# Kernel optimization log

Hardware: AMD Instinct MI355X
Metric: run time of the kernel (lower is better)

Reference implementation:

```python
import jax, jax.numpy as jnp
import numpy as np

B, T, D, H = 4, 2048, 1024, 16
E = D // H  # 64
DH = D // 4  # sensor hidden dim


def setup_inputs() -> dict:
    key = jax.random.key(0)
    ks = jax.random.split(key, 9)
    s = D ** -0.5
    return {
        "x": jax.random.normal(ks[0], (B, T, D), jnp.float32),
        "q_w": jax.random.normal(ks[1], (D, D), jnp.float32) * s,
        "k_w": jax.random.normal(ks[2], (D, D), jnp.float32) * s,
        "v_w": jax.random.normal(ks[3], (D, D), jnp.float32) * s,
        "o_w": jax.random.normal(ks[4], (D, D), jnp.float32) * s,
        "cs_w1": jax.random.normal(ks[5], (DH, D), jnp.float32) * s,
        "cs_b1": jnp.zeros((DH,), jnp.float32),
        "cs_w2": jax.random.normal(ks[6], (H, DH), jnp.float32) * (DH ** -0.5),
        "cs_b2": jnp.zeros((H,), jnp.float32),
        "decay_params": jax.random.normal(ks[7], (H, E), jnp.float32) + 3.0,
    }


def reference(x, q_w, k_w, v_w, o_w, cs_w1, cs_b1, cs_w2, cs_b2, decay_params):
    Bx, Tx, Dx = x.shape
    # projections (torch Linear: y = x @ W.T), split into heads
    q = (x @ q_w.T).reshape(Bx, Tx, H, E)
    k = (x @ k_w.T).reshape(Bx, Tx, H, E)
    v = (x @ v_w.T).reshape(Bx, Tx, H, E)
    # complexity sensor -> per-head scalar in (0,1)
    lc = jax.nn.sigmoid(jnp.tanh(x @ cs_w1.T + cs_b1) @ cs_w2.T + cs_b2)  # [B,T,H]
    base = jax.nn.sigmoid(decay_params)[None, None]                       # [1,1,H,E]
    lam = jnp.clip(base * (1.0 + 0.2 * lc[..., None]), 0.0, 0.9995)       # [B,T,H,E]

    def step(state, inp):
        qt, kt, vt, dt = inp  # each [B,H,E]
        # S(t) = diag(dt) S(t-1) + k_t v_t^T  (decay along key dim e)
        state = state * dt[..., None] + kt[..., None] * vt[:, :, None, :]
        out_t = jnp.einsum('bhe,bhef->bhf', qt, state)
        return state, out_t

    init = jnp.zeros((Bx, H, E, E), x.dtype)
    xs = (jnp.swapaxes(q, 0, 1), jnp.swapaxes(k, 0, 1),
          jnp.swapaxes(v, 0, 1), jnp.swapaxes(lam, 0, 1))  # time-major
    _, ys = jax.lax.scan(step, init, xs)  # ys: [T,B,H,E]
    y = jnp.swapaxes(ys, 0, 1).reshape(Bx, Tx, Dx)
    return y @ o_w.T
```

## Files before the change

### kernel.cpp

```cpp
#include <hip/hip_runtime.h>

#define DEV __device__ __forceinline__
#define MFMA(a, b, c) __builtin_amdgcn_mfma_f32_16x16x32_bf16(a, b, c, 0, 0, 0)

typedef __bf16 bf16x8 __attribute__((ext_vector_type(8)));
typedef float f32x4 __attribute__((ext_vector_type(4)));
typedef unsigned short u16x8 __attribute__((ext_vector_type(8)));

DEV float blo(unsigned u) { return __builtin_bit_cast(float, u << 16); }
DEV float bhi(unsigned u) { return __builtin_bit_cast(float, u & 0xFFFF0000u); }
DEV unsigned short f2b(float f) {
  unsigned u = __builtin_bit_cast(unsigned, f);
  return (unsigned short)((u + 0x7FFFu + ((u >> 16) & 1u)) >> 16);
}
DEV float sigf(float x) { return 1.0f / (1.0f + expf(-x)); }

DEV void llds16(const void* g, void* l) {
  __builtin_amdgcn_global_load_lds(
      (__attribute__((address_space(1))) void*)(void*)g,
      (__attribute__((address_space(3))) void*)l, 16, 0, 0);
}

__global__ __launch_bounds__(256) void cvt_all_kernel(
    const float* __restrict__ x, const float* __restrict__ qw,
    const float* __restrict__ kw, const float* __restrict__ vw,
    const float* __restrict__ cw1, const float* __restrict__ ow,
    unsigned short* __restrict__ XB, unsigned short* __restrict__ WCAT,
    unsigned short* __restrict__ OWB) {
  const int i = blockIdx.x * 256 + threadIdx.x;
  const float* s;
  unsigned short* d;
  if (i < 2097152)      { s = x   + (size_t)i * 4;                 d = XB + (size_t)i * 4; }
  else if (i < 2359296) { size_t j = i - 2097152; s = qw  + j * 4; d = WCAT + j * 4; }
  else if (i < 2621440) { size_t j = i - 2359296; s = kw  + j * 4; d = WCAT + 1048576 + j * 4; }
  else if (i < 2883584) { size_t j = i - 2621440; s = vw  + j * 4; d = WCAT + 2097152 + j * 4; }
  else if (i < 2949120) { size_t j = i - 2883584; s = cw1 + j * 4; d = WCAT + 3145728 + j * 4; }
  else if (i < 3211264) { size_t j = i - 2949120; s = ow  + j * 4; d = OWB + j * 4; }
  else return;
  float4 f = *(const float4*)s;
  ushort4 o;
  o.x = f2b(f.x); o.y = f2b(f.y); o.z = f2b(f.z); o.w = f2b(f.w);
  *(ushort4*)d = o;
}

template <int OUTF>
__global__ __launch_bounds__(256, 2) void gemm_bk64_kernel(
    const unsigned short* __restrict__ A, const unsigned short* __restrict__ B,
    void* __restrict__ Cout, int M, int N, int K, int act_col0,
    const float* __restrict__ bias, int nbn) {
  __shared__ char As[16384];
  __shared__ char Bs[16384];
  const int tid = threadIdx.x;
  const int lane = tid & 63;
  const int w = tid >> 6;
  const int wr = w >> 1, wc = w & 1;
  const int ln15 = lane & 15, hi = lane >> 4;

  const int nwg = gridDim.x, orig = blockIdx.x;
  const int qd = nwg >> 3, rm = nwg & 7;
  const int xcd = orig & 7, loc = orig >> 3;
  const int swz = (xcd < rm ? xcd * (qd + 1) : rm * (qd + 1) + (xcd - rm) * qd) + loc;
  const int bn = swz % nbn, bm = swz / nbn;
  const int m0 = bm * 128, n0 = bn * 128;

  auto stage = [&](const unsigned short* src, int row0, int k0, char* dst) {
#pragma unroll
    for (int j = 0; j < 4; ++j) {
      const int slot = j * 256 + tid;
      const int rr = slot >> 3;
      const int kc = (slot & 7) ^ (rr & 7);
      llds16(src + (size_t)(row0 + rr) * K + k0 + kc * 8, dst + slot * 16);
    }
  };
  auto rd = [&](const char* unit, int row, int ks) -> bf16x8 {
    const int kc = (ks * 4 + hi) ^ (row & 7);
    return *(const bf16x8*)(unit + row * 128 + kc * 16);
  };

  f32x4 acc[4][4] = {};
  const int nk = K >> 6;
  for (int kt = 0; kt < nk; ++kt) {
    stage(A, m0, kt * 64, As);
    stage(B, n0, kt * 64, Bs);
    __syncthreads();
    bf16x8 af[2][4], bf[2][4];
#pragma unroll
    for (int ks = 0; ks < 2; ++ks)
#pragma unroll
      for (int i = 0; i < 4; ++i) {
        af[ks][i] = rd(As, wr * 64 + i * 16 + ln15, ks);
        bf[ks][i] = rd(Bs, wc * 64 + i * 16 + ln15, ks);
      }
#pragma unroll
    for (int i = 0; i < 4; ++i)
#pragma unroll
      for (int j = 0; j < 4; ++j) {
        acc[i][j] = MFMA(af[0][i], bf[0][j], acc[i][j]);
        acc[i][j] = MFMA(af[1][i], bf[1][j], acc[i][j]);
      }
    __syncthreads();
  }
#pragma unroll
  for (int i = 0; i < 4; ++i) {
    const int rowb = m0 + wr * 64 + i * 16 + hi * 4;
#pragma unroll
    for (int j = 0; j < 4; ++j) {
      const int col = n0 + wc * 64 + j * 16 + ln15;
#pragma unroll
      for (int r = 0; r < 4; ++r) {
        float v = acc[i][j][r];
        if (col >= act_col0) v = tanhf(v + bias[col - act_col0]);
        const size_t off = (size_t)(rowb + r) * N + col;
        if (OUTF == 0) ((unsigned short*)Cout)[off] = f2b(v);
        else ((float*)Cout)[off] = v;
      }
    }
  }
}

__global__ __launch_bounds__(256) void sensor2_kernel(
    const unsigned short* __restrict__ QKVH, const float* __restrict__ w2,
    const float* __restrict__ b2, float* __restrict__ LC) {
  const int tid = threadIdx.x;
  const int h = tid & 15, r = tid >> 4;
  const int m = blockIdx.x * 16 + r;
  const unsigned short* hrow = QKVH + (size_t)m * 3328 + 3072;
  const float* wrow = w2 + h * 256;
  float acc = 0.0f;
  for (int d = 0; d < 256; d += 8) {
    uint4 hv = *(const uint4*)(hrow + d);
    float4 wa = *(const float4*)(wrow + d);
    float4 wb = *(const float4*)(wrow + d + 4);
    acc = fmaf(blo(hv.x), wa.x, acc); acc = fmaf(bhi(hv.x), wa.y, acc);
    acc = fmaf(blo(hv.y), wa.z, acc); acc = fmaf(bhi(hv.y), wa.w, acc);
    acc = fmaf(blo(hv.z), wb.x, acc); acc = fmaf(bhi(hv.z), wb.y, acc);
    acc = fmaf(blo(hv.w), wb.z, acc); acc = fmaf(bhi(hv.w), wb.w, acc);
  }
  LC[(size_t)m * 16 + h] = sigf(acc + b2[h]);
}

__global__ __launch_bounds__(256) void scan_passA_kernel(
    const unsigned short* __restrict__ QKVH, const float* __restrict__ LC,
    const float* __restrict__ decay, float* __restrict__ MT, float* __restrict__ P) {
  __shared__ char SH[34304];
  ushort* kL = (ushort*)SH;
  ushort* vL = (ushort*)(SH + 8192);
  char* khT  = SH + 16384;
  char* vT   = SH + 24576;
  float* sigL = (float*)(SH + 32768);
  float* lcL  = (float*)(SH + 33024);
  float* Lp   = (float*)(SH + 33280);

  const int tid = threadIdx.x;
  const int c = blockIdx.x, h = blockIdx.y, b = blockIdx.z;
  const int t0 = c * 64;
#pragma unroll
  for (int i = 0; i < 2; ++i) {
    int idx = i * 256 + tid;
    int row = idx >> 3, ch = idx & 7;
    size_t g = (size_t)(b * 2048 + t0 + row) * 3328 + h * 64 + ch * 8;
    int lb = (i * 256 + (tid >> 6) * 64) * 16;
    llds16(QKVH + g + 1024, (char*)kL + lb);
    llds16(QKVH + g + 2048, (char*)vL + lb);
  }
  if (tid < 64) sigL[tid] = sigf(decay[h * 64 + tid]);
  else if (tid < 128) lcL[tid - 64] = LC[(size_t)(b * 2048 + t0 + tid - 64) * 16 + h];
  __syncthreads();

  const int e = tid & 63, seg = tid >> 6;
  const float sig_e = sigL[e];
  float lp = 1.f;
#pragma unroll
  for (int i = 0; i < 16; ++i)
    lp *= fminf(sig_e * (1.f + 0.2f * lcL[seg * 16 + i]), 0.9995f);
  Lp[seg * 64 + e] = lp;
  __syncthreads();
  float T = 1.f;
#pragma unroll
  for (int sg = 0; sg < 4; ++sg) if (sg > seg) T *= Lp[sg * 64 + e];

  u16x8 ka = {}, kb = {};
  float r = T;
#pragma unroll
  for (int i = 15; i >= 0; --i) {
    int s = seg * 16 + i;
    float lam = fminf(sig_e * (1.f + 0.2f * lcL[s]), 0.9995f);
    float kv = blo((unsigned)kL[s * 64 + e]) * r;
    if (i >= 8) kb[i - 8] = f2b(kv); else ka[i] = f2b(kv);
    r *= lam;
  }
  *(u16x8*)(khT + e * 128 + (((2 * seg + 0) ^ (e & 7)) * 16)) = ka;
  *(u16x8*)(khT + e * 128 + (((2 * seg + 1) ^ (e & 7)) * 16)) = kb;
  if (seg == 0) P[((size_t)((b * 16 + h) * 32 + c)) * 64 + e] = r;

  u16x8 va = {}, vb = {};
#pragma unroll
  for (int i = 0; i < 16; ++i) {
    unsigned short vv = vL[(seg * 16 + i) * 64 + e];
    if (i >= 8) vb[i - 8] = vv; else va[i] = vv;
  }
  *(u16x8*)(vT + e * 128 + (((2 * seg + 0) ^ (e & 7)) * 16)) = va;
  *(u16x8*)(vT + e * 128 + (((2 * seg + 1) ^ (e & 7)) * 16)) = vb;
  __syncthreads();

  const int ln15 = tid & 15, hi = (tid & 63) >> 4, w = tid >> 6;
  auto rd = [&](const char* u, int row, int ks) -> bf16x8 {
    return *(const bf16x8*)(u + row * 128 + (((ks * 4 + hi) ^ (row & 7)) * 16));
  };
  bf16x8 av0 = rd(vT, w * 16 + ln15, 0), av1 = rd(vT, w * 16 + ln15, 1);
  float* Mp = MT + ((size_t)((b * 16 + h) * 32 + c)) * 4096;
#pragma unroll
  for (int er = 0; er < 4; ++er) {
    f32x4 acc = {};
    acc = MFMA(av0, rd(khT, er * 16 + ln15, 0), acc);
    acc = MFMA(av1, rd(khT, er * 16 + ln15, 1), acc);
#pragma unroll
    for (int rr = 0; rr < 4; ++rr)
      Mp[(w * 16 + hi * 4 + rr) * 64 + er * 16 + ln15] = acc[rr];
  }
}

__global__ __launch_bounds__(256) void scan_passB_kernel(
    float* __restrict__ MT, const float* __restrict__ P) {
  const int bh = blockIdx.y;
  const int ef = blockIdx.x * 256 + threadIdx.x;
  const int e = ef & 63;
  const size_t base = (size_t)bh * 32;
  float S = 0.0f;
  for (int c = 0; c < 32; ++c) {
    float* Mp = MT + (base + c) * 4096 + ef;
    const float p = P[(base + c) * 64 + e];
    const float m = *Mp;
    *Mp = S;
    S = fmaf(p, S, m);
  }
}

__global__ __launch_bounds__(256) void scan_passC_kernel(
    const unsigned short* __restrict__ QKVH, const float* __restrict__ LC,
    const float* __restrict__ decay, const float* __restrict__ MT,
    unsigned short* __restrict__ Y) {
  __shared__ char SH[50688];
  ushort* qL = (ushort*)SH;
  ushort* kL = (ushort*)(SH + 8192);
  ushort* vL = (ushort*)(SH + 16384);
  char* qT = SH + 24576;
  char* kT = SH + 32768;
  char* vT = SH + 40960;
  char* Ab   = SH;
  char* sinT = SH + 8192;
  float* sigL = (float*)(SH + 49152);
  float* lcL  = (float*)(SH + 49408);
  float* Lp   = (float*)(SH + 49664);

  const int tid = threadIdx.x;
  const int c = blockIdx.x, h = blockIdx.y, b = blockIdx.z;
  const int t0 = c * 64;
#pragma unroll
  for (int i = 0; i < 2; ++i) {
    int idx = i * 256 + tid;
    int row = idx >> 3, ch = idx & 7;
    size_t g = (size_t)(b * 2048 + t0 + row) * 3328 + h * 64 + ch * 8;
    int lb = (i * 256 + (tid >> 6) * 64) * 16;
    llds16(QKVH + g,        (char*)qL + lb);
    llds16(QKVH + g + 1024, (char*)kL + lb);
    llds16(QKVH + g + 2048, (char*)vL + lb);
  }
  if (tid < 64) sigL[tid] = sigf(decay[h * 64 + tid]);
  else if (tid < 128) lcL[tid - 64] = LC[(size_t)(b * 2048 + t0 + tid - 64) * 16 + h];
  __syncthreads();

  const int e = tid & 63, seg = tid >> 6;
  const float sig_e = sigL[e];
  float lp = 1.f;
#pragma unroll
  for (int i = 0; i < 16; ++i)
    lp *= fminf(sig_e * (1.f + 0.2f * lcL[seg * 16 + i]), 0.9995f);
  Lp[seg * 64 + e] = lp;
  __syncthreads();
  float a = 1.f;
#pragma unroll
  for (int sg = 0; sg < 4; ++sg) if (sg < seg) a *= Lp[sg * 64 + e];

#pragma unroll
  for (int i = 0; i < 16; ++i) {
    int t = seg * 16 + i;
    a *= fminf(sig_e * (1.f + 0.2f * lcL[t]), 0.9995f);
    float qv = blo((unsigned)qL[t * 64 + e]) * a;
    float kv = blo((unsigned)kL[t * 64 + e]) / fmaxf(a, 1e-30f);
    int off = ((e >> 3) ^ (t & 7)) * 16 + (e & 7) * 2;
    *(unsigned short*)(qT + t * 128 + off) = f2b(qv);
    *(unsigned short*)(kT + t * 128 + off) = f2b(kv);
  }
  u16x8 va = {}, vb = {};
#pragma unroll
  for (int i = 0; i < 16; ++i) {
    unsigned short vv = vL[(seg * 16 + i) * 64 + e];
    if (i >= 8) vb[i - 8] = vv; else va[i] = vv;
  }
  *(u16x8*)(vT + e * 128 + (((2 * seg + 0) ^ (e & 7)) * 16)) = va;
  *(u16x8*)(vT + e * 128 + (((2 * seg + 1) ^ (e & 7)) * 16)) = vb;
  __syncthreads();

  const int ln15 = tid & 15, hi = (tid & 63) >> 4, w = tid >> 6;
  auto rd = [&](const char* u, int row, int ks) -> bf16x8 {
    return *(const bf16x8*)(u + row * 128 + (((ks * 4 + hi) ^ (row & 7)) * 16));
  };
  bf16x8 Aq0 = rd(qT, w * 16 + ln15, 0), Aq1 = rd(qT, w * 16 + ln15, 1);
  f32x4 acc1[4];
#pragma unroll
  for (int sr = 0; sr < 4; ++sr) {
    acc1[sr] = (f32x4){0.f, 0.f, 0.f, 0.f};
    if (sr <= w) {
      acc1[sr] = MFMA(Aq0, rd(kT, sr * 16 + ln15, 0), acc1[sr]);
      acc1[sr] = MFMA(Aq1, rd(kT, sr * 16 + ln15, 1), acc1[sr]);
    }
  }
#pragma unroll
  for (int sr = 0; sr < 4; ++sr)
#pragma unroll
    for (int rr = 0; rr < 4; ++rr) {
      int t = w * 16 + hi * 4 + rr;
      int s = sr * 16 + ln15;
      float v = 0.f;
      if (sr <= w && s <= t) v = acc1[sr][rr];
      *(unsigned short*)(Ab + t * 128 + (((s >> 3) ^ (t & 7)) * 16) + (s & 7) * 2) = f2b(v);
    }
  {
    const float* Ms = MT + ((size_t)((b * 16 + h) * 32 + c)) * 4096 + (tid >> 2) * 64 + (tid & 3) * 16;
    const int f2 = tid >> 2, s0 = (tid & 3) * 2;
    u16x8 sa = {}, sb = {};
#pragma unroll
    for (int j = 0; j < 4; ++j) {
      float4 m4 = *(const float4*)(Ms + j * 4);
      if (j < 2) {
        sa[j * 4 + 0] = f2b(m4.x); sa[j * 4 + 1] = f2b(m4.y);
        sa[j * 4 + 2] = f2b(m4.z); sa[j * 4 + 3] = f2b(m4.w);
      } else {
        sb[(j - 2) * 4 + 0] = f2b(m4.x); sb[(j - 2) * 4 + 1] = f2b(m4.y);
        sb[(j - 2) * 4 + 2] = f2b(m4.z); sb[(j - 2) * 4 + 3] = f2b(m4.w);
      }
    }
    *(u16x8*)(sinT + f2 * 128 + (((s0 + 0) ^ (f2 & 7)) * 16)) = sa;
    *(u16x8*)(sinT + f2 * 128 + (((s0 + 1) ^ (f2 & 7)) * 16)) = sb;
  }
  __syncthreads();

  f32x4 accY[4];
#pragma unroll
  for (int fr = 0; fr < 4; ++fr) {
    accY[fr] = (f32x4){0.f, 0.f, 0.f, 0.f};
    accY[fr] = MFMA(Aq0, rd(sinT, fr * 16 + ln15, 0), accY[fr]);
    accY[fr] = MFMA(Aq1, rd(sinT, fr * 16 + ln15, 1), accY[fr]);
  }
  bf16x8 Aa0 = rd(Ab, w * 16 + ln15, 0), Aa1 = rd(Ab, w * 16 + ln15, 1);
#pragma unroll
  for (int fr = 0; fr < 4; ++fr) {
    accY[fr] = MFMA(Aa0, rd(vT, fr * 16 + ln15, 0), accY[fr]);
    accY[fr] = MFMA(Aa1, rd(vT, fr * 16 + ln15, 1), accY[fr]);
  }
#pragma unroll
  for (int fr = 0; fr < 4; ++fr)
#pragma unroll
    for (int rr = 0; rr < 4; ++rr)
      Y[(size_t)(b * 2048 + t0 + w * 16 + hi * 4 + rr) * 1024 + h * 64 + fr * 16 + ln15]
        = f2b(accY[fr][rr]);
}

extern "C" void kernel_launch(void* const* d_in, const int* in_sizes, int n_in,
                              void* d_out, int out_size, void* d_ws, size_t ws_size,
                              hipStream_t stream) {
  (void)in_sizes; (void)n_in; (void)out_size; (void)ws_size;
  const float* x     = (const float*)d_in[0];
  const float* q_w   = (const float*)d_in[1];
  const float* k_w   = (const float*)d_in[2];
  const float* v_w   = (const float*)d_in[3];
  const float* o_w   = (const float*)d_in[4];
  const float* cs_w1 = (const float*)d_in[5];
  const float* cs_b1 = (const float*)d_in[6];
  const float* cs_w2 = (const float*)d_in[7];
  const float* cs_b2 = (const float*)d_in[8];
  const float* decay = (const float*)d_in[9];
  float* out = (float*)d_out;

  char* ws = (char*)d_ws;
  unsigned short* XB   = (unsigned short*)(ws);
  unsigned short* WCAT = (unsigned short*)(ws + 16777216);
  unsigned short* OWB  = (unsigned short*)(ws + 23592960);
  unsigned short* QKVH = (unsigned short*)(ws + 25690112);
  float*          LCb  = (float*)(ws + 80216064);
  float*          MT   = (float*)(ws + 80740352);
  float*          Pb   = (float*)(ws + 114294784);
  unsigned short* YB   = (unsigned short*)(ws + 114819072);

  cvt_all_kernel<<<12544, 256, 0, stream>>>(x, q_w, k_w, v_w, cs_w1, o_w,
                                            XB, WCAT, OWB);

  gemm_bk64_kernel<0><<<1664, 256, 0, stream>>>(XB, WCAT, QKVH, 8192, 3328,
                                                1024, 3072, cs_b1, 26);
  sensor2_kernel<<<512, 256, 0, stream>>>(QKVH, cs_w2, cs_b2, LCb);

  scan_passA_kernel<<<dim3(32, 16, 4), 256, 0, stream>>>(QKVH, LCb, decay, MT, Pb);
  scan_passB_kernel<<<dim3(16, 64), 256, 0, stream>>>(MT, Pb);
  scan_passC_kernel<<<dim3(32, 16, 4), 256, 0, stream>>>(QKVH, LCb, decay, MT, YB);

  gemm_bk64_kernel<1><<<512, 256, 0, stream>>>(YB, OWB, out, 8192, 1024,
                                               1024, 1 << 30, nullptr, 8);
}
```

Baseline: 174.5 us.

## Store inter-chunk states as swizzled bf16 and split sensor hidden output

Pass A now writes the per-chunk state contributions as bf16 in the XOR-swizzled LDS layout instead of fp32. Pass B carries the prefix scan in fp32 but reads and writes bf16, and pass C pulls the states straight into LDS with async global-to-LDS loads, dropping its per-thread fp32 load and convert. The QKV GEMM writes the tanh sensor columns to a separate 256-wide buffer, so QKV rows are 3072 wide. This halves the state traffic and removes conversion work, at the cost of extra rounding: the prefix states are stored in bf16 between chunks.

```diff
diff --git a/kernel.cpp b/kernel.cpp
--- a/kernel.cpp
+++ b/kernel.cpp
@@ -46,8 +46,8 @@
 template <int OUTF>
 __global__ __launch_bounds__(256, 2) void gemm_bk64_kernel(
     const unsigned short* __restrict__ A, const unsigned short* __restrict__ B,
-    void* __restrict__ Cout, int M, int N, int K, int act_col0,
-    const float* __restrict__ bias, int nbn) {
+    void* __restrict__ Cout, unsigned short* __restrict__ Cout2,
+    int K, int ldC, int act_col0, const float* __restrict__ bias, int nbn) {
   __shared__ char As[16384];
   __shared__ char Bs[16384];
   const int tid = threadIdx.x;
@@ -109,22 +109,26 @@
 #pragma unroll
       for (int r = 0; r < 4; ++r) {
         float v = acc[i][j][r];
-        if (col >= act_col0) v = tanhf(v + bias[col - act_col0]);
-        const size_t off = (size_t)(rowb + r) * N + col;
-        if (OUTF == 0) ((unsigned short*)Cout)[off] = f2b(v);
-        else ((float*)Cout)[off] = v;
+        if (col >= act_col0) {
+          v = tanhf(v + bias[col - act_col0]);
+          Cout2[(size_t)(rowb + r) * 256 + (col - act_col0)] = f2b(v);
+        } else {
+          const size_t off = (size_t)(rowb + r) * ldC + col;
+          if (OUTF == 0) ((unsigned short*)Cout)[off] = f2b(v);
+          else ((float*)Cout)[off] = v;
+        }
       }
     }
   }
 }
 
 __global__ __launch_bounds__(256) void sensor2_kernel(
-    const unsigned short* __restrict__ QKVH, const float* __restrict__ w2,
+    const unsigned short* __restrict__ H1, const float* __restrict__ w2,
     const float* __restrict__ b2, float* __restrict__ LC) {
   const int tid = threadIdx.x;
   const int h = tid & 15, r = tid >> 4;
   const int m = blockIdx.x * 16 + r;
-  const unsigned short* hrow = QKVH + (size_t)m * 3328 + 3072;
+  const unsigned short* hrow = H1 + (size_t)m * 256;
   const float* wrow = w2 + h * 256;
   float acc = 0.0f;
   for (int d = 0; d < 256; d += 8) {
@@ -140,8 +144,9 @@
 }
 
 __global__ __launch_bounds__(256) void scan_passA_kernel(
-    const unsigned short* __restrict__ QKVH, const float* __restrict__ LC,
-    const float* __restrict__ decay, float* __restrict__ MT, float* __restrict__ P) {
+    const unsigned short* __restrict__ QKV, const float* __restrict__ LC,
+    const float* __restrict__ decay, unsigned short* __restrict__ MTB,
+    float* __restrict__ P) {
   __shared__ char SH[34304];
   ushort* kL = (ushort*)SH;
   ushort* vL = (ushort*)(SH + 8192);
@@ -158,10 +163,10 @@
   for (int i = 0; i < 2; ++i) {
     int idx = i * 256 + tid;
     int row = idx >> 3, ch = idx & 7;
-    size_t g = (size_t)(b * 2048 + t0 + row) * 3328 + h * 64 + ch * 8;
+    size_t g = (size_t)(b * 2048 + t0 + row) * 3072 + h * 64 + ch * 8;
     int lb = (i * 256 + (tid >> 6) * 64) * 16;
-    llds16(QKVH + g + 1024, (char*)kL + lb);
-    llds16(QKVH + g + 2048, (char*)vL + lb);
+    llds16(QKV + g + 1024, (char*)kL + lb);
+    llds16(QKV + g + 2048, (char*)vL + lb);
   }
   if (tid < 64) sigL[tid] = sigf(decay[h * 64 + tid]);
   else if (tid < 128) lcL[tid - 64] = LC[(size_t)(b * 2048 + t0 + tid - 64) * 16 + h];
@@ -208,37 +213,41 @@
     return *(const bf16x8*)(u + row * 128 + (((ks * 4 + hi) ^ (row & 7)) * 16));
   };
   bf16x8 av0 = rd(vT, w * 16 + ln15, 0), av1 = rd(vT, w * 16 + ln15, 1);
-  float* Mp = MT + ((size_t)((b * 16 + h) * 32 + c)) * 4096;
+  unsigned short* Mp = MTB + ((size_t)((b * 16 + h) * 32 + c)) * 4096;
 #pragma unroll
   for (int er = 0; er < 4; ++er) {
     f32x4 acc = {};
     acc = MFMA(av0, rd(khT, er * 16 + ln15, 0), acc);
     acc = MFMA(av1, rd(khT, er * 16 + ln15, 1), acc);
-#pragma unroll
-    for (int rr = 0; rr < 4; ++rr)
-      Mp[(w * 16 + hi * 4 + rr) * 64 + er * 16 + ln15] = acc[rr];
+    const int e2 = er * 16 + ln15;
+#pragma unroll
+    for (int rr = 0; rr < 4; ++rr) {
+      const int f = w * 16 + hi * 4 + rr;
+      Mp[f * 64 + (((e2 >> 3) ^ (f & 7)) << 3) + (e2 & 7)] = f2b(acc[rr]);
+    }
   }
 }
 
 __global__ __launch_bounds__(256) void scan_passB_kernel(
-    float* __restrict__ MT, const float* __restrict__ P) {
+    unsigned short* __restrict__ MTB, const float* __restrict__ P) {
   const int bh = blockIdx.y;
-  const int ef = blockIdx.x * 256 + threadIdx.x;
-  const int e = ef & 63;
+  const int task = blockIdx.x * 256 + threadIdx.x;
+  const int f = task >> 6, slot = (task >> 3) & 7, pos = task & 7;
+  const int e = ((slot ^ (f & 7)) << 3) | pos;
   const size_t base = (size_t)bh * 32;
   float S = 0.0f;
   for (int c = 0; c < 32; ++c) {
-    float* Mp = MT + (base + c) * 4096 + ef;
+    unsigned short* Mp = MTB + (base + c) * 4096 + task;
     const float p = P[(base + c) * 64 + e];
-    const float m = *Mp;
-    *Mp = S;
+    const float m = blo((unsigned)*Mp);
+    *Mp = f2b(S);
     S = fmaf(p, S, m);
   }
 }
 
 __global__ __launch_bounds__(256) void scan_passC_kernel(
-    const unsigned short* __restrict__ QKVH, const float* __restrict__ LC,
-    const float* __restrict__ decay, const float* __restrict__ MT,
+    const unsigned short* __restrict__ QKV, const float* __restrict__ LC,
+    const float* __restrict__ decay, const unsigned short* __restrict__ MTB,
     unsigned short* __restrict__ Y) {
   __shared__ char SH[50688];
   ushort* qL = (ushort*)SH;
@@ -260,11 +269,11 @@
   for (int i = 0; i < 2; ++i) {
     int idx = i * 256 + tid;
     int row = idx >> 3, ch = idx & 7;
-    size_t g = (size_t)(b * 2048 + t0 + row) * 3328 + h * 64 + ch * 8;
+    size_t g = (size_t)(b * 2048 + t0 + row) * 3072 + h * 64 + ch * 8;
     int lb = (i * 256 + (tid >> 6) * 64) * 16;
-    llds16(QKVH + g,        (char*)qL + lb);
-    llds16(QKVH + g + 1024, (char*)kL + lb);
-    llds16(QKVH + g + 2048, (char*)vL + lb);
+    llds16(QKV + g,        (char*)qL + lb);
+    llds16(QKV + g + 1024, (char*)kL + lb);
+    llds16(QKV + g + 2048, (char*)vL + lb);
   }
   if (tid < 64) sigL[tid] = sigf(decay[h * 64 + tid]);
   else if (tid < 128) lcL[tid - 64] = LC[(size_t)(b * 2048 + t0 + tid - 64) * 16 + h];
@@ -302,6 +311,12 @@
   *(u16x8*)(vT + e * 128 + (((2 * seg + 1) ^ (e & 7)) * 16)) = vb;
   __syncthreads();
 
+  {
+    const unsigned short* Ms = MTB + ((size_t)((b * 16 + h) * 32 + c)) * 4096;
+#pragma unroll
+    for (int i = 0; i < 2; ++i)
+      llds16(Ms + (size_t)(i * 256 + tid) * 8, sinT + (i * 256 + (tid >> 6) * 64) * 16);
+  }
   const int ln15 = tid & 15, hi = (tid & 63) >> 4, w = tid >> 6;
   auto rd = [&](const char* u, int row, int ks) -> bf16x8 {
     return *(const bf16x8*)(u + row * 128 + (((ks * 4 + hi) ^ (row & 7)) * 16));
@@ -326,24 +341,7 @@
       if (sr <= w && s <= t) v = acc1[sr][rr];
       *(unsigned short*)(Ab + t * 128 + (((s >> 3) ^ (t & 7)) * 16) + (s & 7) * 2) = f2b(v);
     }
-  {
-    const float* Ms = MT + ((size_t)((b * 16 + h) * 32 + c)) * 4096 + (tid >> 2) * 64 + (tid & 3) * 16;
-    const int f2 = tid >> 2, s0 = (tid & 3) * 2;
-    u16x8 sa = {}, sb = {};
-#pragma unroll
-    for (int j = 0; j < 4; ++j) {
-      float4 m4 = *(const float4*)(Ms + j * 4);
-      if (j < 2) {
-        sa[j * 4 + 0] = f2b(m4.x); sa[j * 4 + 1] = f2b(m4.y);
-        sa[j * 4 + 2] = f2b(m4.z); sa[j * 4 + 3] = f2b(m4.w);
-      } else {
-        sb[(j - 2) * 4 + 0] = f2b(m4.x); sb[(j - 2) * 4 + 1] = f2b(m4.y);
-        sb[(j - 2) * 4 + 2] = f2b(m4.z); sb[(j - 2) * 4 + 3] = f2b(m4.w);
-      }
-    }
-    *(u16x8*)(sinT + f2 * 128 + (((s0 + 0) ^ (f2 & 7)) * 16)) = sa;
-    *(u16x8*)(sinT + f2 * 128 + (((s0 + 1) ^ (f2 & 7)) * 16)) = sb;
-  }
+  bf16x8 Aa0 = rd(Ab, w * 16 + ln15, 0), Aa1 = rd(Ab, w * 16 + ln15, 1);
   __syncthreads();
 
   f32x4 accY[4];
@@ -352,10 +350,6 @@
     accY[fr] = (f32x4){0.f, 0.f, 0.f, 0.f};
     accY[fr] = MFMA(Aq0, rd(sinT, fr * 16 + ln15, 0), accY[fr]);
     accY[fr] = MFMA(Aq1, rd(sinT, fr * 16 + ln15, 1), accY[fr]);
-  }
-  bf16x8 Aa0 = rd(Ab, w * 16 + ln15, 0), Aa1 = rd(Ab, w * 16 + ln15, 1);
-#pragma unroll
-  for (int fr = 0; fr < 4; ++fr) {
     accY[fr] = MFMA(Aa0, rd(vT, fr * 16 + ln15, 0), accY[fr]);
     accY[fr] = MFMA(Aa1, rd(vT, fr * 16 + ln15, 1), accY[fr]);
   }
@@ -387,23 +381,24 @@
   unsigned short* XB   = (unsigned short*)(ws);
   unsigned short* WCAT = (unsigned short*)(ws + 16777216);
   unsigned short* OWB  = (unsigned short*)(ws + 23592960);
-  unsigned short* QKVH = (unsigned short*)(ws + 25690112);
+  unsigned short* QKV  = (unsigned short*)(ws + 25690112);
+  unsigned short* H1   = (unsigned short*)(ws + 76021760);
   float*          LCb  = (float*)(ws + 80216064);
-  float*          MT   = (float*)(ws + 80740352);
-  float*          Pb   = (float*)(ws + 114294784);
-  unsigned short* YB   = (unsigned short*)(ws + 114819072);
+  unsigned short* MTB  = (unsigned short*)(ws + 80740352);
+  float*          Pb   = (float*)(ws + 97517568);
+  unsigned short* YB   = (unsigned short*)(ws + 98041856);
 
   cvt_all_kernel<<<12544, 256, 0, stream>>>(x, q_w, k_w, v_w, cs_w1, o_w,
                                             XB, WCAT, OWB);
 
-  gemm_bk64_kernel<0><<<1664, 256, 0, stream>>>(XB, WCAT, QKVH, 8192, 3328,
-                                                1024, 3072, cs_b1, 26);
-  sensor2_kernel<<<512, 256, 0, stream>>>(QKVH, cs_w2, cs_b2, LCb);
-
-  scan_passA_kernel<<<dim3(32, 16, 4), 256, 0, stream>>>(QKVH, LCb, decay, MT, Pb);
-  scan_passB_kernel<<<dim3(16, 64), 256, 0, stream>>>(MT, Pb);
-  scan_passC_kernel<<<dim3(32, 16, 4), 256, 0, stream>>>(QKVH, LCb, decay, MT, YB);
-
-  gemm_bk64_kernel<1><<<512, 256, 0, stream>>>(YB, OWB, out, 8192, 1024,
-                                               1024, 1 << 30, nullptr, 8);
-}
+  gemm_bk64_kernel<0><<<1664, 256, 0, stream>>>(XB, WCAT, QKV, H1,
+                                                1024, 3072, 3072, cs_b1, 26);
+  sensor2_kernel<<<512, 256, 0, stream>>>(H1, cs_w2, cs_b2, LCb);
+
+  scan_passA_kernel<<<dim3(32, 16, 4), 256, 0, stream>>>(QKV, LCb, decay, MTB, Pb);
+  scan_passB_kernel<<<dim3(16, 64), 256, 0, stream>>>(MTB, Pb);
+  scan_passC_kernel<<<dim3(32, 16, 4), 256, 0, stream>>>(QKV, LCb, decay, MTB, YB);
+
+  gemm_bk64_kernel<1><<<512, 256, 0, stream>>>(YB, OWB, out, nullptr,
+                                               1024, 1024, 1 << 30, nullptr, 8);
+}
```

Result: faster. 169.6 us (-2.8%).
